# Kernel optimization log

Hardware: AMD Instinct MI355X
Metric: run time of the kernel (lower is better)

The kernel has to match this reference:

```python
import jax, jax.numpy as jnp
import numpy as np

EPS = 1e-5  # torch LayerNorm default

def _ln(x, w, b):
    mu = jnp.mean(x, axis=-1, keepdims=True)
    var = jnp.mean((x - mu) ** 2, axis=-1, keepdims=True)
    return (x - mu) * jax.lax.rsqrt(var + EPS) * w + b

def setup_inputs() -> dict:
    B, C, P, D = 256, 256, 256, 256  # broadcasting in final add requires B==P==C
    key = jax.random.key(0)
    ks = jax.random.split(key, 10)
    d_rsqrt = D ** -0.5
    return {
        "x": jax.random.normal(ks[0], (B, C), dtype=jnp.float32),
        "prev_cell_out": jax.random.normal(ks[1], (P, D), dtype=jnp.float32),
        "feature_emb_weight": jax.random.uniform(ks[2], (C, D), minval=-d_rsqrt, maxval=d_rsqrt),
        "feature_emb_bias": jax.random.uniform(ks[3], (1, C, D), minval=-d_rsqrt, maxval=d_rsqrt),
        "ln_emb_w": jnp.ones((D,), jnp.float32), "ln_emb_b": jnp.zeros((D,), jnp.float32),
        "ln_col_w": jnp.ones((D,), jnp.float32), "ln_col_b": jnp.zeros((D,), jnp.float32),
        "ln_prompt_w": jnp.ones((D,), jnp.float32), "ln_prompt_b": jnp.zeros((D,), jnp.float32),
        "dense_imp_w": jax.random.normal(ks[4], (D, 2 * D)) * (2 * D) ** -0.5,  # torch Linear weight [out,in]
        "dense_imp_b": jnp.zeros((D,), jnp.float32),
        "emb_column": jax.random.normal(ks[5], (C, D)) * 0.01,
        "emb_prompt": jax.random.normal(ks[6], (P, D)) * 0.01,
        "expand_weight": jax.random.normal(ks[7], (P, 1)),  # dense_expand.weight [n_prompts, 1]
        "expand_bias": jax.random.normal(ks[8], (P,)) * 0.01,
    }

def reference(x, prev_cell_out, feature_emb_weight, feature_emb_bias,
              ln_emb_w, ln_emb_b, ln_col_w, ln_col_b, ln_prompt_w, ln_prompt_b,
              dense_imp_w, dense_imp_b, emb_column, emb_prompt,
              expand_weight, expand_bias):
    # addcmul: bias + x[...,None] * weight -> [B, C, D]
    x_emb = _ln(jax.nn.relu(feature_emb_bias + x[..., None] * feature_emb_weight), ln_emb_w, ln_emb_b)
    # prompt path (unbatched): [P, 2D] -> [P, D]
    xp_in = jnp.concatenate([_ln(emb_prompt, ln_prompt_w, ln_prompt_b), prev_cell_out], axis=-1)
    x_prompt = xp_in @ dense_imp_w.T + dense_imp_b + emb_prompt
    x_col = _ln(emb_column, ln_col_w, ln_col_b)  # [C, D]
    mask = jax.nn.softmax(x_prompt @ x_col.T, axis=-1)  # [P, C]
    # einsum 'pc,bcd->bpd'
    x_out = jnp.einsum('pc,bcd->bpd', mask, x_emb)
    # 'pc,bcd,pa->bpd' with a==1 is the same contraction scaled per-prompt by expand_weight[p,0]
    x_out = x_out * (1.0 + expand_weight[:, 0])[None, :, None]
    # 'pc,p->pc' then unsqueeze(0).unsqueeze(-1): [1, P, C, 1]; broadcasts [B,P,D] -> [1,B,P,D]
    bias_term = (mask * expand_bias[:, None])[None, :, :, None]
    return x_out + bias_term  # [1, B, P, D] (B==P==C)
```

## Files before the change

kernel.cpp:

```cpp
#include <hip/hip_runtime.h>
#include <cstdint>

typedef _Float16 half8 __attribute__((ext_vector_type(8)));
typedef float f32x4 __attribute__((ext_vector_type(4)));

#define LN_EPS 1e-5f

__device__ __forceinline__ float dot4(float4 a, float4 b) {
  return a.x*b.x + a.y*b.y + a.z*b.z + a.w*b.w;
}

__global__ __launch_bounds__(256) void k_pre(
    const float* __restrict__ x, const float* __restrict__ few, const float* __restrict__ feb,
    const float* __restrict__ emb_pr, const float* __restrict__ lnp_w, const float* __restrict__ lnp_b,
    const float* __restrict__ prev, const float* __restrict__ W, const float* __restrict__ Wb,
    const float* __restrict__ emb_col, const float* __restrict__ lnc_w, const float* __restrict__ lnc_b,
    float2* __restrict__ stats2, float* __restrict__ mask_f32, _Float16* __restrict__ mask_f16)
{
  __shared__ __align__(16) struct {
    float xin[512];
    float xq[256];
    float sc[256];
    float wr1[4], wr2[4];
  } sm;

  int t = threadIdx.x, w = t >> 6, lane = t & 63;

  if (blockIdx.x >= 256) {
    int bid = blockIdx.x - 256;
    int b = bid >> 3;
    int cg = (bid & 7) * 4 + w;
    int c0 = cg * 8;
    float xv[8];
    #pragma unroll
    for (int j = 0; j < 8; ++j) xv[j] = x[b*256 + c0 + j];
    float s1[8], s2[8];
    #pragma unroll
    for (int j = 0; j < 8; ++j) { s1[j] = 0.f; s2[j] = 0.f; }
    #pragma unroll
    for (int j = 0; j < 8; ++j) {
      float4 fw = ((const float4*)few)[(c0+j)*64 + lane];
      float4 fb = ((const float4*)feb)[(c0+j)*64 + lane];
      float4 v;
      v.x = fmaxf(fb.x + xv[j]*fw.x, 0.f);
      v.y = fmaxf(fb.y + xv[j]*fw.y, 0.f);
      v.z = fmaxf(fb.z + xv[j]*fw.z, 0.f);
      v.w = fmaxf(fb.w + xv[j]*fw.w, 0.f);
      s1[j] += v.x + v.y + v.z + v.w;
      s2[j] += v.x*v.x + v.y*v.y + v.z*v.z + v.w*v.w;
    }
    #pragma unroll
    for (int o = 32; o > 0; o >>= 1) {
      #pragma unroll
      for (int j = 0; j < 8; ++j) { s1[j] += __shfl_xor(s1[j], o); s2[j] += __shfl_xor(s2[j], o); }
    }
    float mu[8], rs[8];
    #pragma unroll
    for (int j = 0; j < 8; ++j) {
      mu[j] = s1[j] * (1.0f/256.0f);
      float var = s2[j] * (1.0f/256.0f) - mu[j]*mu[j];
      rs[j] = rsqrtf(var + LN_EPS);
    }
    float muv = mu[0], rsv = rs[0];
    #pragma unroll
    for (int j = 1; j < 8; ++j) {
      muv = (lane == j) ? mu[j] : muv;
      rsv = (lane == j) ? rs[j] : rsv;
    }
    if (lane < 8) stats2[b*256 + c0 + lane] = make_float2(muv, rsv);
    return;
  }

  int p = blockIdx.x;
  int q = t & 3, g = t >> 2;

  {
    float4 v = ((const float4*)emb_pr)[p*64 + lane];
    float s1 = v.x + v.y + v.z + v.w;
    float s2 = v.x*v.x + v.y*v.y + v.z*v.z + v.w*v.w;
    #pragma unroll
    for (int o = 32; o > 0; o >>= 1) { s1 += __shfl_xor(s1, o); s2 += __shfl_xor(s2, o); }
    float mu = s1 * (1.0f/256.0f);
    float var = s2 * (1.0f/256.0f) - mu*mu;
    float rsv = rsqrtf(var + LN_EPS);
    float4 w4 = ((const float4*)lnp_w)[lane];
    float4 b4 = ((const float4*)lnp_b)[lane];
    float4 y;
    y.x = (v.x-mu)*rsv*w4.x + b4.x;  y.y = (v.y-mu)*rsv*w4.y + b4.y;
    y.z = (v.z-mu)*rsv*w4.z + b4.z;  y.w = (v.w-mu)*rsv*w4.w + b4.w;
    if (w == 0) {
      ((float4*)sm.xin)[lane] = y;
      ((float4*)sm.xin)[64 + lane] = ((const float4*)prev)[p*64 + lane];
    }
  }
  __syncthreads();

  {
    float acc[4] = {0.f, 0.f, 0.f, 0.f};
    #pragma unroll 4
    for (int j = 0; j < 32; ++j) {
      int k4 = j*4 + q;
      float4 xv = ((const float4*)sm.xin)[k4];
      #pragma unroll
      for (int pp = 0; pp < 4; ++pp) {
        int d = pp*64 + g;
        float4 wv = ((const float4*)W)[d*128 + k4];
        acc[pp] += dot4(wv, xv);
      }
    }
    #pragma unroll
    for (int pp = 0; pp < 4; ++pp) {
      acc[pp] += __shfl_xor(acc[pp], 1);
      acc[pp] += __shfl_xor(acc[pp], 2);
    }
    if (q == 0) {
      #pragma unroll
      for (int pp = 0; pp < 4; ++pp) {
        int d = pp*64 + g;
        sm.xq[d] = acc[pp] + Wb[d] + emb_pr[p*256 + d];
      }
    }
  }
  __syncthreads();

  {
    float s1[4] = {0,0,0,0}, s2[4] = {0,0,0,0};
    #pragma unroll 4
    for (int j = 0; j < 16; ++j) {
      int k4 = j*4 + q;
      #pragma unroll
      for (int pp = 0; pp < 4; ++pp) {
        float4 v = ((const float4*)emb_col)[(pp*64+g)*64 + k4];
        s1[pp] += v.x + v.y + v.z + v.w;
        s2[pp] += v.x*v.x + v.y*v.y + v.z*v.z + v.w*v.w;
      }
    }
    float mu[4], rs[4];
    #pragma unroll
    for (int pp = 0; pp < 4; ++pp) {
      s1[pp] += __shfl_xor(s1[pp], 1);  s1[pp] += __shfl_xor(s1[pp], 2);
      s2[pp] += __shfl_xor(s2[pp], 1);  s2[pp] += __shfl_xor(s2[pp], 2);
      mu[pp] = s1[pp] * (1.0f/256.0f);
      float var = s2[pp] * (1.0f/256.0f) - mu[pp]*mu[pp];
      rs[pp] = rsqrtf(var + LN_EPS);
    }
    float acc[4] = {0.f, 0.f, 0.f, 0.f};
    #pragma unroll 4
    for (int j = 0; j < 16; ++j) {
      int k4 = j*4 + q;
      float4 lw4 = ((const float4*)lnc_w)[k4];
      float4 lb4 = ((const float4*)lnc_b)[k4];
      float4 xv = ((const float4*)sm.xq)[k4];
      #pragma unroll
      for (int pp = 0; pp < 4; ++pp) {
        float4 v = ((const float4*)emb_col)[(pp*64+g)*64 + k4];
        float4 nc;
        nc.x = (v.x-mu[pp])*rs[pp]*lw4.x + lb4.x;
        nc.y = (v.y-mu[pp])*rs[pp]*lw4.y + lb4.y;
        nc.z = (v.z-mu[pp])*rs[pp]*lw4.z + lb4.z;
        nc.w = (v.w-mu[pp])*rs[pp]*lw4.w + lb4.w;
        acc[pp] += dot4(nc, xv);
      }
    }
    #pragma unroll
    for (int pp = 0; pp < 4; ++pp) {
      acc[pp] += __shfl_xor(acc[pp], 1);
      acc[pp] += __shfl_xor(acc[pp], 2);
    }
    if (q == 0) {
      #pragma unroll
      for (int pp = 0; pp < 4; ++pp) sm.sc[pp*64 + g] = acc[pp];
    }
  }
  __syncthreads();

  {
    float val = sm.sc[t];
    float m0 = val;
    #pragma unroll
    for (int o = 32; o > 0; o >>= 1) m0 = fmaxf(m0, __shfl_xor(m0, o));
    if (lane == 0) sm.wr1[w] = m0;
    __syncthreads();
    float M = fmaxf(fmaxf(sm.wr1[0], sm.wr1[1]), fmaxf(sm.wr1[2], sm.wr1[3]));
    float e = expf(val - M);
    float s = e;
    #pragma unroll
    for (int o = 32; o > 0; o >>= 1) s += __shfl_xor(s, o);
    if (lane == 0) sm.wr2[w] = s;
    __syncthreads();
    float S = sm.wr2[0] + sm.wr2[1] + sm.wr2[2] + sm.wr2[3];
    float mv = e / S;
    mask_f32[p*256 + t] = mv;
    mask_f16[p*256 + t] = (_Float16)mv;
  }
}

__global__ __launch_bounds__(256) void k_main(
    const float* __restrict__ x, const float* __restrict__ few, const float* __restrict__ feb,
    const float* __restrict__ ln_emb_w, const float* __restrict__ ln_emb_b,
    const float2* __restrict__ stats2,
    const _Float16* __restrict__ mask_f16, const float* __restrict__ mask_f32,
    const float* __restrict__ ew, const float* __restrict__ eb,
    float* __restrict__ out)
{
  __shared__ __align__(16) _Float16 Bs[8 * 64 * 8];
  __shared__ float xrow[256];
  __shared__ float2 srow[256];

  int t = threadIdx.x, w = t >> 6, lane = t & 63;
  int lm = lane & 15, quad = lane >> 4;
  int b = blockIdx.x >> 2;
  int ds = (blockIdx.x & 3) * 64;
  int dl = t & 63;

  xrow[t] = x[b*256 + t];
  srow[t] = stats2[b*256 + t];
  float lwv = ln_emb_w[ds + dl];
  float lbv = ln_emb_b[ds + dl];

  f32x4 acc[4][4];
  #pragma unroll
  for (int i = 0; i < 4; ++i)
    #pragma unroll
    for (int j = 0; j < 4; ++j)
      acc[i][j] = (f32x4){0.f, 0.f, 0.f, 0.f};

  __syncthreads();

  for (int kb = 0; kb < 4; ++kb) {
    half8 h0, h1;
    #pragma unroll
    for (int j = 0; j < 16; ++j) {
      int cl = kb*64 + w*16 + j;
      float fw = few[cl*256 + ds + dl];
      float fb = feb[cl*256 + ds + dl];
      float xc = xrow[cl];
      float2 st = srow[cl];
      float v = fmaxf(fb + xc*fw, 0.f);
      _Float16 hh = (_Float16)((v - st.x) * st.y * lwv + lbv);
      if (j < 8) h0[j] = hh; else h1[j-8] = hh;
    }
    *(half8*)(Bs + ((w*2 + 0)*64 + dl)*8) = h0;
    *(half8*)(Bs + ((w*2 + 1)*64 + dl)*8) = h1;
    __syncthreads();

    #pragma unroll
    for (int ks = 0; ks < 2; ++ks) {
      half8 af[4], bf[4];
      #pragma unroll
      for (int mt = 0; mt < 4; ++mt)
        af[mt] = *(const half8*)(mask_f16 + (size_t)(w*64 + mt*16 + lm)*256 + kb*64 + ks*32 + quad*8);
      #pragma unroll
      for (int nt = 0; nt < 4; ++nt)
        bf[nt] = *(const half8*)(Bs + ((ks*4 + quad)*64 + nt*16 + lm)*8);
      #pragma unroll
      for (int mt = 0; mt < 4; ++mt)
        #pragma unroll
        for (int nt = 0; nt < 4; ++nt)
          acc[mt][nt] = __builtin_amdgcn_mfma_f32_16x16x32_f16(af[mt], bf[nt], acc[mt][nt], 0, 0, 0);
    }
    __syncthreads();
  }

  float ebv = eb[b];
  #pragma unroll
  for (int mt = 0; mt < 4; ++mt) {
    float sp[4], tb[4];
    #pragma unroll
    for (int r = 0; r < 4; ++r) {
      int p = w*64 + mt*16 + quad*4 + r;
      sp[r] = 1.0f + ew[p];
      tb[r] = mask_f32[b*256 + p] * ebv;
    }
    #pragma unroll
    for (int nt = 0; nt < 4; ++nt) {
      int d = ds + nt*16 + lm;
      #pragma unroll
      for (int r = 0; r < 4; ++r) {
        int p = w*64 + mt*16 + quad*4 + r;
        out[((size_t)b << 16) + ((size_t)p << 8) + d] = acc[mt][nt][r] * sp[r] + tb[r];
      }
    }
  }
}

extern "C" void kernel_launch(void* const* d_in, const int* in_sizes, int n_in,
                              void* d_out, int out_size, void* d_ws, size_t ws_size,
                              hipStream_t stream) {
  const float* x        = (const float*)d_in[0];
  const float* prev     = (const float*)d_in[1];
  const float* few      = (const float*)d_in[2];
  const float* feb      = (const float*)d_in[3];
  const float* ln_emb_w = (const float*)d_in[4];
  const float* ln_emb_b = (const float*)d_in[5];
  const float* ln_col_w = (const float*)d_in[6];
  const float* ln_col_b = (const float*)d_in[7];
  const float* ln_pr_w  = (const float*)d_in[8];
  const float* ln_pr_b  = (const float*)d_in[9];
  const float* dimp_w   = (const float*)d_in[10];
  const float* dimp_b   = (const float*)d_in[11];
  const float* emb_col  = (const float*)d_in[12];
  const float* emb_pr   = (const float*)d_in[13];
  const float* ew       = (const float*)d_in[14];
  const float* eb       = (const float*)d_in[15];
  float* out = (float*)d_out;

  char* wsb = (char*)d_ws;
  float2*   ws_stats  = (float2*)(wsb);
  float*    ws_mask   = (float*)(wsb + 524288);
  _Float16* ws_mask_h = (_Float16*)(wsb + 786432);

  k_pre<<<dim3(256 + 2048), dim3(256), 0, stream>>>(
      x, few, feb,
      emb_pr, ln_pr_w, ln_pr_b, prev, dimp_w, dimp_b,
      emb_col, ln_col_w, ln_col_b,
      ws_stats, ws_mask, ws_mask_h);
  k_main<<<dim3(1024), dim3(256), 0, stream>>>(
      x, few, feb, ln_emb_w, ln_emb_b,
      ws_stats, ws_mask_h, ws_mask, ew, eb, out);
}
```

Measured before the change: 159.8 us.

## Restructure LN stats per column and double-buffer B tile in main GEMM

The stats path in k_pre is reorganised so each block handles one column c. It stages that column's weight and bias rows in shared memory, and each thread computes the LayerNorm mean and rstd for one batch row, which cuts the block count from 2304 to 512. k_main splits the D dimension into 32-wide slices, giving 2048 blocks and a smaller accumulator, and adds a launch-bounds occupancy hint. It also double-buffers the shared B tile, prefetching the next k-chunk's global loads into registers while the MFMAs run, which removes one barrier per iteration. The trade-off is more redundant reads of the mask A-operand across blocks and strided writes to the stats array.

Result: slower. 174.3 us (+9.0%).

```diff
diff --git a/kernel.cpp b/kernel.cpp
--- a/kernel.cpp
+++ b/kernel.cpp
@@ -23,51 +23,32 @@
     float sc[256];
     float wr1[4], wr2[4];
   } sm;
+  __shared__ __align__(16) float fw_s[256];
+  __shared__ __align__(16) float fb_s[256];
 
   int t = threadIdx.x, w = t >> 6, lane = t & 63;
 
   if (blockIdx.x >= 256) {
-    int bid = blockIdx.x - 256;
-    int b = bid >> 3;
-    int cg = (bid & 7) * 4 + w;
-    int c0 = cg * 8;
-    float xv[8];
-    #pragma unroll
-    for (int j = 0; j < 8; ++j) xv[j] = x[b*256 + c0 + j];
-    float s1[8], s2[8];
-    #pragma unroll
-    for (int j = 0; j < 8; ++j) { s1[j] = 0.f; s2[j] = 0.f; }
-    #pragma unroll
-    for (int j = 0; j < 8; ++j) {
-      float4 fw = ((const float4*)few)[(c0+j)*64 + lane];
-      float4 fb = ((const float4*)feb)[(c0+j)*64 + lane];
-      float4 v;
-      v.x = fmaxf(fb.x + xv[j]*fw.x, 0.f);
-      v.y = fmaxf(fb.y + xv[j]*fw.y, 0.f);
-      v.z = fmaxf(fb.z + xv[j]*fw.z, 0.f);
-      v.w = fmaxf(fb.w + xv[j]*fw.w, 0.f);
-      s1[j] += v.x + v.y + v.z + v.w;
-      s2[j] += v.x*v.x + v.y*v.y + v.z*v.z + v.w*v.w;
-    }
-    #pragma unroll
-    for (int o = 32; o > 0; o >>= 1) {
-      #pragma unroll
-      for (int j = 0; j < 8; ++j) { s1[j] += __shfl_xor(s1[j], o); s2[j] += __shfl_xor(s2[j], o); }
-    }
-    float mu[8], rs[8];
-    #pragma unroll
-    for (int j = 0; j < 8; ++j) {
-      mu[j] = s1[j] * (1.0f/256.0f);
-      float var = s2[j] * (1.0f/256.0f) - mu[j]*mu[j];
-      rs[j] = rsqrtf(var + LN_EPS);
-    }
-    float muv = mu[0], rsv = rs[0];
-    #pragma unroll
-    for (int j = 1; j < 8; ++j) {
-      muv = (lane == j) ? mu[j] : muv;
-      rsv = (lane == j) ? rs[j] : rsv;
-    }
-    if (lane < 8) stats2[b*256 + c0 + lane] = make_float2(muv, rsv);
+    int c = blockIdx.x - 256;
+    fw_s[t] = few[c*256 + t];
+    fb_s[t] = feb[c*256 + t];
+    __syncthreads();
+    float xv = x[t*256 + c];
+    float s1 = 0.f, s2 = 0.f;
+    #pragma unroll 16
+    for (int d4 = 0; d4 < 64; ++d4) {
+      float4 fw = ((const float4*)fw_s)[d4];
+      float4 fb = ((const float4*)fb_s)[d4];
+      float v0 = fmaxf(fb.x + xv*fw.x, 0.f);
+      float v1 = fmaxf(fb.y + xv*fw.y, 0.f);
+      float v2 = fmaxf(fb.z + xv*fw.z, 0.f);
+      float v3 = fmaxf(fb.w + xv*fw.w, 0.f);
+      s1 += v0 + v1 + v2 + v3;
+      s2 += v0*v0 + v1*v1 + v2*v2 + v3*v3;
+    }
+    float mu = s1 * (1.0f/256.0f);
+    float var = s2 * (1.0f/256.0f) - mu*mu;
+    stats2[t*256 + c] = make_float2(mu, rsqrtf(var + LN_EPS));
     return;
   }
 
@@ -195,7 +176,7 @@
   }
 }
 
-__global__ __launch_bounds__(256) void k_main(
+__global__ __launch_bounds__(256, 4) void k_main(
     const float* __restrict__ x, const float* __restrict__ few, const float* __restrict__ feb,
     const float* __restrict__ ln_emb_w, const float* __restrict__ ln_emb_b,
     const float2* __restrict__ stats2,
@@ -203,66 +184,90 @@
     const float* __restrict__ ew, const float* __restrict__ eb,
     float* __restrict__ out)
 {
-  __shared__ __align__(16) _Float16 Bs[8 * 64 * 8];
+  __shared__ __align__(16) _Float16 Bs[2][8 * 32 * 8];
   __shared__ float xrow[256];
-  __shared__ float2 srow[256];
-
-  int t = threadIdx.x, w = t >> 6, lane = t & 63;
-  int lm = lane & 15, quad = lane >> 4;
-  int b = blockIdx.x >> 2;
-  int ds = (blockIdx.x & 3) * 64;
-  int dl = t & 63;
+  __shared__ __align__(8) float2 srow[256];
+
+  const int t = threadIdx.x, w = t >> 6, lane = t & 63;
+  const int lm = lane & 15, quad = lane >> 4;
+  const int b  = blockIdx.x >> 3;
+  const int ds = (blockIdx.x & 7) * 32;
+  const int g  = t >> 5, dl = t & 31;
+  const int d  = ds + dl;
 
   xrow[t] = x[b*256 + t];
   srow[t] = stats2[b*256 + t];
-  float lwv = ln_emb_w[ds + dl];
-  float lbv = ln_emb_b[ds + dl];
-
-  f32x4 acc[4][4];
+  const float lwv = ln_emb_w[d];
+  const float lbv = ln_emb_b[d];
+
+  f32x4 acc[4][2];
   #pragma unroll
-  for (int i = 0; i < 4; ++i)
-    #pragma unroll
-    for (int j = 0; j < 4; ++j)
-      acc[i][j] = (f32x4){0.f, 0.f, 0.f, 0.f};
-
+  for (int i = 0; i < 4; ++i) {
+    acc[i][0] = (f32x4){0.f, 0.f, 0.f, 0.f};
+    acc[i][1] = (f32x4){0.f, 0.f, 0.f, 0.f};
+  }
+
+  float fwv[8], fbv[8];
+  #pragma unroll
+  for (int j = 0; j < 8; ++j) {
+    int cl = g*8 + j;
+    fwv[j] = few[cl*256 + d];
+    fbv[j] = feb[cl*256 + d];
+  }
+  __syncthreads();
+  {
+    half8 h;
+    #pragma unroll
+    for (int j = 0; j < 8; ++j) {
+      int cl = g*8 + j;
+      float2 st = srow[cl];
+      float v = fmaxf(fbv[j] + xrow[cl]*fwv[j], 0.f);
+      h[j] = (_Float16)((v - st.x) * st.y * lwv + lbv);
+    }
+    *(half8*)(&Bs[0][(g*32 + dl)*8]) = h;
+  }
   __syncthreads();
 
   for (int kb = 0; kb < 4; ++kb) {
-    half8 h0, h1;
-    #pragma unroll
-    for (int j = 0; j < 16; ++j) {
-      int cl = kb*64 + w*16 + j;
-      float fw = few[cl*256 + ds + dl];
-      float fb = feb[cl*256 + ds + dl];
-      float xc = xrow[cl];
-      float2 st = srow[cl];
-      float v = fmaxf(fb + xc*fw, 0.f);
-      _Float16 hh = (_Float16)((v - st.x) * st.y * lwv + lbv);
-      if (j < 8) h0[j] = hh; else h1[j-8] = hh;
-    }
-    *(half8*)(Bs + ((w*2 + 0)*64 + dl)*8) = h0;
-    *(half8*)(Bs + ((w*2 + 1)*64 + dl)*8) = h1;
-    __syncthreads();
-
+    if (kb < 3) {
+      #pragma unroll
+      for (int j = 0; j < 8; ++j) {
+        int cl = (kb+1)*64 + g*8 + j;
+        fwv[j] = few[cl*256 + d];
+        fbv[j] = feb[cl*256 + d];
+      }
+    }
+    const _Float16* Bcur = &Bs[kb & 1][0];
     #pragma unroll
     for (int ks = 0; ks < 2; ++ks) {
-      half8 af[4], bf[4];
+      half8 af[4], bf[2];
       #pragma unroll
       for (int mt = 0; mt < 4; ++mt)
         af[mt] = *(const half8*)(mask_f16 + (size_t)(w*64 + mt*16 + lm)*256 + kb*64 + ks*32 + quad*8);
       #pragma unroll
-      for (int nt = 0; nt < 4; ++nt)
-        bf[nt] = *(const half8*)(Bs + ((ks*4 + quad)*64 + nt*16 + lm)*8);
+      for (int nt = 0; nt < 2; ++nt)
+        bf[nt] = *(const half8*)(Bcur + ((ks*4 + quad)*32 + nt*16 + lm)*8);
       #pragma unroll
       for (int mt = 0; mt < 4; ++mt)
         #pragma unroll
-        for (int nt = 0; nt < 4; ++nt)
+        for (int nt = 0; nt < 2; ++nt)
           acc[mt][nt] = __builtin_amdgcn_mfma_f32_16x16x32_f16(af[mt], bf[nt], acc[mt][nt], 0, 0, 0);
     }
-    __syncthreads();
-  }
-
-  float ebv = eb[b];
+    if (kb < 3) {
+      half8 h;
+      #pragma unroll
+      for (int j = 0; j < 8; ++j) {
+        int cl = (kb+1)*64 + g*8 + j;
+        float2 st = srow[cl];
+        float v = fmaxf(fbv[j] + xrow[cl]*fwv[j], 0.f);
+        h[j] = (_Float16)((v - st.x) * st.y * lwv + lbv);
+      }
+      *(half8*)(&Bs[(kb+1) & 1][(g*32 + dl)*8]) = h;
+      __syncthreads();
+    }
+  }
+
+  const float ebv = eb[b];
   #pragma unroll
   for (int mt = 0; mt < 4; ++mt) {
     float sp[4], tb[4];
@@ -273,12 +278,12 @@
       tb[r] = mask_f32[b*256 + p] * ebv;
     }
     #pragma unroll
-    for (int nt = 0; nt < 4; ++nt) {
-      int d = ds + nt*16 + lm;
+    for (int nt = 0; nt < 2; ++nt) {
+      int dd = ds + nt*16 + lm;
       #pragma unroll
       for (int r = 0; r < 4; ++r) {
         int p = w*64 + mt*16 + quad*4 + r;
-        out[((size_t)b << 16) + ((size_t)p << 8) + d] = acc[mt][nt][r] * sp[r] + tb[r];
+        out[((size_t)b << 16) + ((size_t)p << 8) + dd] = acc[mt][nt][r] * sp[r] + tb[r];
       }
     }
   }
@@ -310,12 +315,12 @@
   float*    ws_mask   = (float*)(wsb + 524288);
   _Float16* ws_mask_h = (_Float16*)(wsb + 786432);
 
-  k_pre<<<dim3(256 + 2048), dim3(256), 0, stream>>>(
+  k_pre<<<dim3(512), dim3(256), 0, stream>>>(
       x, few, feb,
       emb_pr, ln_pr_w, ln_pr_b, prev, dimp_w, dimp_b,
       emb_col, ln_col_w, ln_col_b,
       ws_stats, ws_mask, ws_mask_h);
-  k_main<<<dim3(1024), dim3(256), 0, stream>>>(
+  k_main<<<dim3(2048), dim3(256), 0, stream>>>(
       x, few, feb, ln_emb_w, ln_emb_b,
       ws_stats, ws_mask_h, ws_mask, ew, eb, out);
 }
```

## Double-buffer LDS tile and prefetch next feature-embedding slice during MFMA

Applied to the files above, without the earlier changes.

Turns the k_main K-loop into a two-stage software pipeline. The next chunk's feature_emb weight and bias loads are issued into registers before the MFMAs on the current chunk, and the next B tile is built into an alternate shared buffer afterwards, leaving one barrier per iteration instead of two. The goal is to hide global-load latency behind tensor work. It costs 32 extra registers per thread, which could lower occupancy, and doubles the B-tile shared memory.

Result: faster. 149.5 us (-6.5%).

```diff
diff --git a/kernel.cpp b/kernel.cpp
--- a/kernel.cpp
+++ b/kernel.cpp
@@ -203,20 +203,21 @@
     const float* __restrict__ ew, const float* __restrict__ eb,
     float* __restrict__ out)
 {
-  __shared__ __align__(16) _Float16 Bs[8 * 64 * 8];
+  __shared__ __align__(16) _Float16 Bs[2][8 * 64 * 8];
   __shared__ float xrow[256];
-  __shared__ float2 srow[256];
-
-  int t = threadIdx.x, w = t >> 6, lane = t & 63;
-  int lm = lane & 15, quad = lane >> 4;
-  int b = blockIdx.x >> 2;
-  int ds = (blockIdx.x & 3) * 64;
-  int dl = t & 63;
+  __shared__ __align__(8) float2 srow[256];
+
+  const int t = threadIdx.x, w = t >> 6, lane = t & 63;
+  const int lm = lane & 15, quad = lane >> 4;
+  const int b  = blockIdx.x >> 2;
+  const int ds = (blockIdx.x & 3) * 64;
+  const int dl = t & 63;
+  const int d  = ds + dl;
 
   xrow[t] = x[b*256 + t];
   srow[t] = stats2[b*256 + t];
-  float lwv = ln_emb_w[ds + dl];
-  float lbv = ln_emb_b[ds + dl];
+  const float lwv = ln_emb_w[d];
+  const float lbv = ln_emb_b[d];
 
   f32x4 acc[4][4];
   #pragma unroll
@@ -225,25 +226,39 @@
     for (int j = 0; j < 4; ++j)
       acc[i][j] = (f32x4){0.f, 0.f, 0.f, 0.f};
 
-  __syncthreads();
-
-  for (int kb = 0; kb < 4; ++kb) {
+  float fwv[16], fbv[16];
+  #pragma unroll
+  for (int j = 0; j < 16; ++j) {
+    int cl = w*16 + j;
+    fwv[j] = few[cl*256 + d];
+    fbv[j] = feb[cl*256 + d];
+  }
+  __syncthreads();
+  {
     half8 h0, h1;
     #pragma unroll
     for (int j = 0; j < 16; ++j) {
-      int cl = kb*64 + w*16 + j;
-      float fw = few[cl*256 + ds + dl];
-      float fb = feb[cl*256 + ds + dl];
-      float xc = xrow[cl];
+      int cl = w*16 + j;
       float2 st = srow[cl];
-      float v = fmaxf(fb + xc*fw, 0.f);
+      float v = fmaxf(fbv[j] + xrow[cl]*fwv[j], 0.f);
       _Float16 hh = (_Float16)((v - st.x) * st.y * lwv + lbv);
       if (j < 8) h0[j] = hh; else h1[j-8] = hh;
     }
-    *(half8*)(Bs + ((w*2 + 0)*64 + dl)*8) = h0;
-    *(half8*)(Bs + ((w*2 + 1)*64 + dl)*8) = h1;
-    __syncthreads();
-
+    *(half8*)(&Bs[0][((w*2 + 0)*64 + dl)*8]) = h0;
+    *(half8*)(&Bs[0][((w*2 + 1)*64 + dl)*8]) = h1;
+  }
+  __syncthreads();
+
+  for (int kb = 0; kb < 4; ++kb) {
+    if (kb < 3) {
+      #pragma unroll
+      for (int j = 0; j < 16; ++j) {
+        int cl = (kb+1)*64 + w*16 + j;
+        fwv[j] = few[cl*256 + d];
+        fbv[j] = feb[cl*256 + d];
+      }
+    }
+    const _Float16* Bcur = &Bs[kb & 1][0];
     #pragma unroll
     for (int ks = 0; ks < 2; ++ks) {
       half8 af[4], bf[4];
@@ -252,17 +267,30 @@
         af[mt] = *(const half8*)(mask_f16 + (size_t)(w*64 + mt*16 + lm)*256 + kb*64 + ks*32 + quad*8);
       #pragma unroll
       for (int nt = 0; nt < 4; ++nt)
-        bf[nt] = *(const half8*)(Bs + ((ks*4 + quad)*64 + nt*16 + lm)*8);
+        bf[nt] = *(const half8*)(Bcur + ((ks*4 + quad)*64 + nt*16 + lm)*8);
       #pragma unroll
       for (int mt = 0; mt < 4; ++mt)
         #pragma unroll
         for (int nt = 0; nt < 4; ++nt)
           acc[mt][nt] = __builtin_amdgcn_mfma_f32_16x16x32_f16(af[mt], bf[nt], acc[mt][nt], 0, 0, 0);
     }
-    __syncthreads();
-  }
-
-  float ebv = eb[b];
+    if (kb < 3) {
+      half8 h0, h1;
+      #pragma unroll
+      for (int j = 0; j < 16; ++j) {
+        int cl = (kb+1)*64 + w*16 + j;
+        float2 st = srow[cl];
+        float v = fmaxf(fbv[j] + xrow[cl]*fwv[j], 0.f);
+        _Float16 hh = (_Float16)((v - st.x) * st.y * lwv + lbv);
+        if (j < 8) h0[j] = hh; else h1[j-8] = hh;
+      }
+      *(half8*)(&Bs[(kb+1) & 1][((w*2 + 0)*64 + dl)*8]) = h0;
+      *(half8*)(&Bs[(kb+1) & 1][((w*2 + 1)*64 + dl)*8]) = h1;
+      __syncthreads();
+    }
+  }
+
+  const float ebv = eb[b];
   #pragma unroll
   for (int mt = 0; mt < 4; ++mt) {
     float sp[4], tb[4];
@@ -274,11 +302,11 @@
     }
     #pragma unroll
     for (int nt = 0; nt < 4; ++nt) {
-      int d = ds + nt*16 + lm;
+      int dd = ds + nt*16 + lm;
       #pragma unroll
       for (int r = 0; r < 4; ++r) {
         int p = w*64 + mt*16 + quad*4 + r;
-        out[((size_t)b << 16) + ((size_t)p << 8) + d] = acc[mt][nt][r] * sp[r] + tb[r];
+        out[((size_t)b << 16) + ((size_t)p << 8) + dd] = acc[mt][nt][r] * sp[r] + tb[r];
       }
     }
   }
```
